# Performance work log

Measured on AMD Instinct MI355X. Metric: run time of the kernel, lower is better.

Reference implementation:

```python
import jax, jax.numpy as jnp
import numpy as np

ALPHA = 0.2       # LeakyReLU negative slope
NEG = -9.0e15     # masking value used by the torch module

def setup_inputs() -> dict:
    key = jax.random.key(0)
    k1, k2, k3, k4, k5, k6 = jax.random.split(key, 6)
    bs, N, F_out, Fx = 32, 1024, 128, 8
    inputs = {
        "input": jax.random.normal(k1, (bs, N, 1), dtype=jnp.float32),
        "adj": jax.random.randint(k2, (N, N), 0, 2, dtype=jnp.int32),
        "ext_input": jax.random.normal(k3, (bs, N, Fx), dtype=jnp.float32),
        "side_input": jax.random.normal(k4, (bs, N, 1), dtype=jnp.float32),
        "W": jax.random.normal(k5, (1, F_out), dtype=jnp.float32) * (1.414 * (6.0 / (1 + F_out)) ** 0.5),
        "a": jax.random.normal(k6, (2 * F_out, 1), dtype=jnp.float32) * (1.414 * (6.0 / (2 * F_out + 1)) ** 0.5),
    }
    return inputs

def reference(input, adj, ext_input, side_input, W, a):
    # ext_input / side_input are reshaped but unused in the original forward.
    bs = input.shape[0]
    x = input.reshape(bs, -1, 1)                      # (bs, N, 1)
    h = jnp.matmul(x, W)                              # (bs, N, F)
    Fo = W.shape[1]
    a1 = a[:Fo, 0]                                    # (F,)
    a2 = a[Fo:, 0]                                    # (F,)
    # Decomposed concat-score: e[b,i,j] = leakyrelu(h_i . a1 + h_j . a2)
    s1 = jnp.einsum('bnf,f->bn', h, a1)               # (bs, N)
    s2 = jnp.einsum('bnf,f->bn', h, a2)               # (bs, N)
    e = jax.nn.leaky_relu(s1[:, :, None] + s2[:, None, :], negative_slope=ALPHA)  # (bs, N, N)
    mask = (adj > 0)[None, :, :]                      # broadcast over batch (adj.repeat)
    att = jnp.where(mask, e, NEG)
    att = jnp.where(att > 0, att, NEG)                # second positivity mask in the module
    att = jax.nn.softmax(att, axis=2)                 # (bs, N, N)
    h_prime = jnp.matmul(att, h)                      # (bs, N, F)
    return jax.nn.elu(h_prime)                        # concat=True branch
```

## Files before the change

### kernel.cpp

```cpp
#include <hip/hip_runtime.h>

constexpr int N  = 1024;
constexpr int BS = 32;
constexpr int FO = 128;

template <int ctrl, int rmask>
__device__ __forceinline__ float dpp_add(float x) {
  int y = __builtin_amdgcn_update_dpp(0, __float_as_int(x), ctrl, rmask, 0xf, true);
  return x + __int_as_float(y);
}

__device__ __forceinline__ float wave_sum_bcast(float x) {
  x = dpp_add<0x111, 0xf>(x);
  x = dpp_add<0x112, 0xf>(x);
  x = dpp_add<0x114, 0xf>(x);
  x = dpp_add<0x118, 0xf>(x);
  x = dpp_add<0x142, 0xa>(x);
  x = dpp_add<0x143, 0xc>(x);
  return __int_as_float(__builtin_amdgcn_readlane(__float_as_int(x), 63));
}

__global__ __launch_bounds__(64) void gat_fused(
    const float* __restrict__ x, const int* __restrict__ adj,
    const float* __restrict__ W, const float* __restrict__ a,
    float* __restrict__ out) {
  const int i    = blockIdx.x;
  const int lane = threadIdx.x;

  const float wl = W[lane], wh = W[lane + 64];
  const float c1 = wave_sum_bcast(wl * a[lane] + wh * a[lane + 64]);
  const float c2 = wave_sum_bcast(wl * a[FO + lane] + wh * a[FO + 64 + lane]);

  const float2 w2 = reinterpret_cast<const float2*>(W)[lane];

  float adjf[16];
  const int4* arow = reinterpret_cast<const int4*>(adj + (size_t)i * N);
#pragma unroll
  for (int k = 0; k < 4; ++k) {
    int4 aq = arow[lane + 64 * k];
    adjf[k * 4 + 0] = aq.x > 0 ? 1.f : 0.f;
    adjf[k * 4 + 1] = aq.y > 0 ? 1.f : 0.f;
    adjf[k * 4 + 2] = aq.z > 0 ? 1.f : 0.f;
    adjf[k * 4 + 3] = aq.w > 0 ? 1.f : 0.f;
  }

  const int b0 = blockIdx.y * (BS / 4);
  for (int b = b0; b < b0 + BS / 4; ++b) {
    const float* xb = x + b * N;
    const float thr = -c1 * xb[i];
    float Z = 0.f, Wm = 0.f, S = 0.f;
    const float4* xrow = reinterpret_cast<const float4*>(xb);
#pragma unroll
    for (int k = 0; k < 4; ++k) {
      float4 xq = xrow[lane + 64 * k];
      float xv[4] = {xq.x, xq.y, xq.z, xq.w};
#pragma unroll
      for (int m = 0; m < 4; ++m) {
        float xj = xv[m];
        S += xj;
        float w = c2 * xj;
        float u = __expf(w);
        float uu = ((w > thr) ? adjf[k * 4 + m] : 0.f) * u;
        Z += uu;
        Wm = fmaf(uu, xj, Wm);
      }
    }
    Z  = wave_sum_bcast(Z);
    Wm = wave_sum_bcast(Wm);
    S  = wave_sum_bcast(S);
    float t = (Z > 0.f) ? (Wm / Z) : (S * (1.f / N));

    float z0 = t * w2.x, z1 = t * w2.y;
    float2 r;
    r.x = z0 > 0.f ? z0 : __expf(z0) - 1.f;
    r.y = z1 > 0.f ? z1 : __expf(z1) - 1.f;
    reinterpret_cast<float2*>(out + ((size_t)b * N + i) * FO)[lane] = r;
  }
}

extern "C" void kernel_launch(void* const* d_in, const int* in_sizes, int n_in,
                              void* d_out, int out_size, void* d_ws, size_t ws_size,
                              hipStream_t stream) {
  const float* x   = (const float*)d_in[0];
  const int*   adj = (const int*)d_in[1];
  const float* W   = (const float*)d_in[4];
  const float* a   = (const float*)d_in[5];
  float* out = (float*)d_out;

  hipLaunchKernelGGL(gat_fused, dim3(N, 4), dim3(64), 0, stream,
                     x, adj, W, a, out);
}
```

Before: 84.18 us.

## Precompute exp table and row sums in a prep kernel, split batch finer

Adds a prep kernel that computes exp(c2*x) for every batch element, the per-batch sums of x and the constants c1/c2, storing them in workspace. The main kernel then reads the exp table instead of recomputing exp per (i,j) pair, drops the per-row sum reduction, and splits the batch dimension over 8 blocks instead of 4 with an unrolled loop. This trades redundant transcendental work for extra memory reads of the table and a second kernel launch.

```diff
diff --git a/kernel.cpp b/kernel.cpp
--- a/kernel.cpp
+++ b/kernel.cpp
@@ -3,6 +3,10 @@
 constexpr int N  = 1024;
 constexpr int BS = 32;
 constexpr int FO = 128;
+
+constexpr int TAB_OFF  = 0;
+constexpr int SUMX_OFF = BS * N;
+constexpr int C12_OFF  = SUMX_OFF + BS;
 
 template <int ctrl, int rmask>
 __device__ __forceinline__ float dpp_add(float x) {
@@ -20,16 +24,42 @@
   return __int_as_float(__builtin_amdgcn_readlane(__float_as_int(x), 63));
 }
 
-__global__ __launch_bounds__(64) void gat_fused(
+__global__ __launch_bounds__(256) void gat_prep(
+    const float* __restrict__ x, const float* __restrict__ W,
+    const float* __restrict__ a, float* __restrict__ ws) {
+  const int b    = blockIdx.x;
+  const int tid  = threadIdx.x;
+  const int lane = tid & 63;
+
+  const float wl = W[lane], wh = W[lane + 64];
+  const float c1 = wave_sum_bcast(wl * a[lane] + wh * a[lane + 64]);
+  const float c2 = wave_sum_bcast(wl * a[FO + lane] + wh * a[FO + 64 + lane]);
+
+  float4 xq = reinterpret_cast<const float4*>(x + (size_t)b * N)[tid];
+  float4 e;
+  e.x = __expf(c2 * xq.x);
+  e.y = __expf(c2 * xq.y);
+  e.z = __expf(c2 * xq.z);
+  e.w = __expf(c2 * xq.w);
+  reinterpret_cast<float4*>(ws + TAB_OFF)[b * (N / 4) + tid] = e;
+
+  float s = wave_sum_bcast(xq.x + xq.y + xq.z + xq.w);
+  __shared__ float ls[4];
+  if (lane == 0) ls[tid >> 6] = s;
+  __syncthreads();
+  if (tid == 0) ws[SUMX_OFF + b] = ls[0] + ls[1] + ls[2] + ls[3];
+  if (b == 0 && tid == 0) { ws[C12_OFF] = c1; ws[C12_OFF + 1] = c2; }
+}
+
+__global__ __launch_bounds__(64) void gat_main(
     const float* __restrict__ x, const int* __restrict__ adj,
-    const float* __restrict__ W, const float* __restrict__ a,
+    const float* __restrict__ W, const float* __restrict__ ws,
     float* __restrict__ out) {
   const int i    = blockIdx.x;
   const int lane = threadIdx.x;
 
-  const float wl = W[lane], wh = W[lane + 64];
-  const float c1 = wave_sum_bcast(wl * a[lane] + wh * a[lane + 64]);
-  const float c2 = wave_sum_bcast(wl * a[FO + lane] + wh * a[FO + 64 + lane]);
+  const float c1 = ws[C12_OFF];
+  const float c2 = ws[C12_OFF + 1];
 
   const float2 w2 = reinterpret_cast<const float2*>(W)[lane];
 
@@ -44,31 +74,31 @@
     adjf[k * 4 + 3] = aq.w > 0 ? 1.f : 0.f;
   }
 
-  const int b0 = blockIdx.y * (BS / 4);
-  for (int b = b0; b < b0 + BS / 4; ++b) {
+  const int b0 = blockIdx.y * (BS / 8);
+#pragma unroll
+  for (int b = b0; b < b0 + BS / 8; ++b) {
     const float* xb = x + b * N;
     const float thr = -c1 * xb[i];
-    float Z = 0.f, Wm = 0.f, S = 0.f;
+    float Z = 0.f, Wm = 0.f;
     const float4* xrow = reinterpret_cast<const float4*>(xb);
+    const float4* Erow = reinterpret_cast<const float4*>(ws + TAB_OFF + (size_t)b * N);
 #pragma unroll
     for (int k = 0; k < 4; ++k) {
       float4 xq = xrow[lane + 64 * k];
+      float4 eq = Erow[lane + 64 * k];
       float xv[4] = {xq.x, xq.y, xq.z, xq.w};
+      float ev[4] = {eq.x, eq.y, eq.z, eq.w};
 #pragma unroll
       for (int m = 0; m < 4; ++m) {
-        float xj = xv[m];
-        S += xj;
-        float w = c2 * xj;
-        float u = __expf(w);
-        float uu = ((w > thr) ? adjf[k * 4 + m] : 0.f) * u;
-        Z += uu;
-        Wm = fmaf(uu, xj, Wm);
+        float w   = c2 * xv[m];
+        float sel = (w > thr) ? (adjf[k * 4 + m] * ev[m]) : 0.f;
+        Z += sel;
+        Wm = fmaf(sel, xv[m], Wm);
       }
     }
     Z  = wave_sum_bcast(Z);
     Wm = wave_sum_bcast(Wm);
-    S  = wave_sum_bcast(S);
-    float t = (Z > 0.f) ? (Wm / Z) : (S * (1.f / N));
+    float t = (Z > 0.f) ? (Wm / Z) : (ws[SUMX_OFF + b] * (1.f / N));
 
     float z0 = t * w2.x, z1 = t * w2.y;
     float2 r;
@@ -85,8 +115,10 @@
   const int*   adj = (const int*)d_in[1];
   const float* W   = (const float*)d_in[4];
   const float* a   = (const float*)d_in[5];
+  float* ws  = (float*)d_ws;
   float* out = (float*)d_out;
 
-  hipLaunchKernelGGL(gat_fused, dim3(N, 4), dim3(64), 0, stream,
-                     x, adj, W, a, out);
+  hipLaunchKernelGGL(gat_prep, dim3(BS), dim3(256), 0, stream, x, W, a, ws);
+  hipLaunchKernelGGL(gat_main, dim3(N, 8), dim3(64), 0, stream,
+                     x, adj, W, ws, out);
 }
```

Measured after the change: 84.11 us. No clear change (-0.1%).
